# Kernel optimization log

Measured on AMD Instinct MI355X. Metric: run time of the kernel, lower is better.

Reference implementation:

```python
import jax, jax.numpy as jnp
import numpy as np

DIM = 192
NH = 6
HD = DIM // NH            # 32
SCALE = HD ** -0.5
HID = int(DIM * 4.0)      # 768
EPS = 1e-5


def _ln(x, g, b):
    m = jnp.mean(x, axis=-1, keepdims=True)
    v = jnp.mean((x - m) ** 2, axis=-1, keepdims=True)
    return (x - m) * jax.lax.rsqrt(v + EPS) * g + b


def setup_inputs() -> dict:
    key = jax.random.key(0)
    ks = jax.random.split(key, 6)
    H = W = T = 48
    B = 1
    L = H * W * T
    return {
        "x": jax.random.normal(ks[0], (B, L, DIM), jnp.float32),
        "norm1_g": jnp.ones((DIM,), jnp.float32),
        "norm1_b": jnp.zeros((DIM,), jnp.float32),
        "qkv_w": jax.random.normal(ks[1], (3 * DIM, DIM), jnp.float32) * 0.02,
        "qkv_b": jnp.zeros((3 * DIM,), jnp.float32),
        "proj_w": jax.random.normal(ks[2], (DIM, DIM), jnp.float32) * 0.02,
        "proj_b": jnp.zeros((DIM,), jnp.float32),
        "norm2_g": jnp.ones((DIM,), jnp.float32),
        "norm2_b": jnp.zeros((DIM,), jnp.float32),
        "fc1_w": jax.random.normal(ks[3], (HID, DIM), jnp.float32) * 0.02,
        "fc1_b": jnp.zeros((HID,), jnp.float32),
        "fc2_w": jax.random.normal(ks[4], (DIM, HID), jnp.float32) * 0.02,
        "fc2_b": jnp.zeros((DIM,), jnp.float32),
        "H": H, "W": W, "T": T,
    }


def reference(x, norm1_g, norm1_b, qkv_w, qkv_b, proj_w, proj_b,
              norm2_g, norm2_b, fc1_w, fc1_b, fc2_w, fc2_b, H, W, T):
    B, L, C = x.shape
    shortcut = x
    h = _ln(x, norm1_g, norm1_b)
    # axial_dims='12' -> extra_dim=3: permute to (B, T, H, W, C), attend over H*W
    h = h.reshape(B, H, W, T, C).transpose(0, 3, 1, 2, 4).reshape(B * T, H * W, C)
    B_, N, _ = h.shape
    qkv = h @ qkv_w.T + qkv_b                                   # (B_, N, 3C)
    # faithful reproduction of the module's unusual reshape mixing batch into head dim
    qkv = qkv.transpose(1, 0, 2).reshape(1, N, 3, NH, B_ * HD).transpose(2, 0, 3, 1, 4)
    q, k, v = qkv[0] * SCALE, qkv[1], qkv[2]                    # (1, NH, N, B_*HD)
    attn = jax.nn.softmax(jnp.einsum('ohnd,ohmd->ohnm', q, k), axis=-1)
    o = jnp.einsum('ohnm,ohmd->ohnd', attn, v)                  # (1, NH, N, B_*HD)
    o = o.transpose(0, 2, 1, 3).reshape(B_, N, C)
    o = o @ proj_w.T + proj_b
    o = o.reshape(B, H * W * T, C)                              # module does NOT undo the permute
    x1 = shortcut + o
    m = _ln(x1, norm2_g, norm2_b)
    m = jax.nn.gelu(m @ fc1_w.T + fc1_b, approximate=False) @ fc2_w.T + fc2_b
    return x1 + m
```

## Files before the change

### kernel.cpp

```cpp
#include <hip/hip_runtime.h>

typedef __bf16 bf16_t;
typedef __attribute__((ext_vector_type(8))) __bf16 bf16x8;
typedef __attribute__((ext_vector_type(4))) float f32x4;

__device__ __forceinline__ float gelu_exact(float x) {
    return 0.5f * x * (1.0f + erff(x * 0.70710678118654752f));
}

template<int BM, int BN, int EPI, int SWZ>
__global__ __launch_bounds__(256)
void mgemm(const bf16_t* __restrict__ A, int lda, long aBatch,
           const bf16_t* __restrict__ B, int ldb, long bBatch,
           bf16_t* __restrict__ C, int ldc, long cBatch,
           const float* __restrict__ bias, int K,
           float* __restrict__ Cf, const float* __restrict__ resid)
{
    constexpr int MR = BM / 32;
    constexpr int NR = BN / 32;
    constexpr int LPT = BM / 32 + BN / 32;
    __shared__ __align__(16) bf16_t As[2][BM * 64];
    __shared__ __align__(16) bf16_t Bs[2][BN * 64];
    const int t    = threadIdx.x;
    const int w    = t >> 6;
    const int lane = t & 63;
    const int wr   = w >> 1, wc = w & 1;

    unsigned bx = blockIdx.x, by = blockIdx.y, bz = blockIdx.z;
    if constexpr (SWZ) {
        const unsigned gx = gridDim.x, gy = gridDim.y, gz = gridDim.z;
        unsigned lin = (bz * gy + by) * gx + bx;
        const unsigned cpx = (gx * gy * gz) >> 3;
        lin = (lin & 7) * cpx + (lin >> 3);
        bx = lin % gx; lin /= gx;
        by = lin % gy; bz = lin / gy;
    }

    const long n0 = (long)bx * BN;
    const long m0 = (long)by * BM;
    A += (long)bz * aBatch;
    B += (long)bz * bBatch;
    if constexpr (EPI != 3) C += (long)bz * cBatch;

    f32x4 acc[MR][NR] = {};

    const int srow8  = t >> 3;
    const int schunk = (t & 7) ^ (srow8 & 7);
    const int lrow = lane & 15;
    const int kq4  = lane >> 4;

    auto stage = [&](int buf, int k0) {
        #pragma unroll
        for (int c = 0; c < BM / 32; ++c) {
            const bf16_t* src = A + (m0 + c * 32 + srow8) * (long)lda + (k0 + schunk * 8);
            __builtin_amdgcn_global_load_lds(
                (__attribute__((address_space(1))) void*)(bf16_t*)src,
                (__attribute__((address_space(3))) void*)(As[buf] + c * 2048 + w * 512),
                16, 0, 0);
        }
        #pragma unroll
        for (int c = 0; c < BN / 32; ++c) {
            const bf16_t* src = B + (n0 + c * 32 + srow8) * (long)ldb + (k0 + schunk * 8);
            __builtin_amdgcn_global_load_lds(
                (__attribute__((address_space(1))) void*)(bf16_t*)src,
                (__attribute__((address_space(3))) void*)(Bs[buf] + c * 2048 + w * 512),
                16, 0, 0);
        }
    };

    const int nt = K >> 6;
    stage(0, 0);
    int cur = 0;
    for (int kt = 0; kt < nt; ++kt) {
        if (kt + 1 < nt) {
            stage(cur ^ 1, (kt + 1) << 6);
            if constexpr (LPT == 8)
                asm volatile("s_waitcnt vmcnt(8)" ::: "memory");
            else
                asm volatile("s_waitcnt vmcnt(6)" ::: "memory");
        } else {
            asm volatile("s_waitcnt vmcnt(0)" ::: "memory");
        }
        __builtin_amdgcn_s_barrier();

        bf16x8 af[MR][2], bfr[NR][2];
        #pragma unroll
        for (int i = 0; i < MR; ++i) {
            const int row = wr * (BM / 2) + i * 16 + lrow;
            #pragma unroll
            for (int ks = 0; ks < 2; ++ks) {
                const int ch = (ks * 4 + kq4) ^ (row & 7);
                af[i][ks] = *(const bf16x8*)(As[cur] + row * 64 + ch * 8);
            }
        }
        #pragma unroll
        for (int j = 0; j < NR; ++j) {
            const int row = wc * (BN / 2) + j * 16 + lrow;
            #pragma unroll
            for (int ks = 0; ks < 2; ++ks) {
                const int ch = (ks * 4 + kq4) ^ (row & 7);
                bfr[j][ks] = *(const bf16x8*)(Bs[cur] + row * 64 + ch * 8);
            }
        }
        #pragma unroll
        for (int ks = 0; ks < 2; ++ks)
            #pragma unroll
            for (int i = 0; i < MR; ++i)
                #pragma unroll
                for (int j = 0; j < NR; ++j)
                    acc[i][j] = __builtin_amdgcn_mfma_f32_16x16x32_bf16(
                        af[i][ks], bfr[j][ks], acc[i][j], 0, 0, 0);

        asm volatile("s_waitcnt lgkmcnt(0)" ::: "memory");
        __builtin_amdgcn_s_barrier();
        cur ^= 1;
    }

    const int ccol  = lane & 15;
    const int crow4 = (lane >> 4) * 4;
    #pragma unroll
    for (int i = 0; i < MR; ++i) {
        long rowb = m0 + wr * (BM / 2) + i * 16 + crow4;
        #pragma unroll
        for (int j = 0; j < NR; ++j) {
            long col = n0 + wc * (BN / 2) + j * 16 + ccol;
            #pragma unroll
            for (int r = 0; r < 4; ++r) {
                float v = acc[i][j][r];
                long row = rowb + r;
                if constexpr (EPI == 0) {
                    C[row * ldc + col] = (bf16_t)v;
                } else if constexpr (EPI == 1) {
                    C[row * ldc + col] = (bf16_t)(v + bias[col]);
                } else if constexpr (EPI == 2) {
                    C[row * ldc + col] = (bf16_t)gelu_exact(v + bias[col]);
                } else {
                    long idx = row * ldc + col;
                    Cf[idx] = resid[idx] + v + bias[col];
                }
            }
        }
    }
}

__global__ __launch_bounds__(256)
void transpose_v(const bf16_t* __restrict__ Y, bf16_t* __restrict__ Vt)
{
    __shared__ bf16_t tile[64][80];
    const int h  = blockIdx.z;
    const int e0 = blockIdx.x * 64;
    const int m0 = blockIdx.y * 64;
    const int t  = threadIdx.x;
    const int lr = t >> 3;
    const int lc8 = t & 7;

    #pragma unroll
    for (int i = 0; i < 64; i += 32) {
        int row = lr + i;
        bf16x8 vv = *(const bf16x8*)(Y + (long)(m0 + row) * 27648 + 18432 + h * 1536 + e0 + lc8 * 8);
        int cs = lc8 ^ (row >> 3);
        *(bf16x8*)&tile[row][cs * 8] = vv;
    }
    __syncthreads();
    #pragma unroll
    for (int i = 0; i < 64; i += 32) {
        int er = lr + i;
        bf16x8 vv;
        #pragma unroll
        for (int j = 0; j < 8; ++j) {
            int row = lc8 * 8 + j;
            int cs = (er >> 3) ^ lc8;
            vv[j] = tile[row][cs * 8 + (er & 7)];
        }
        *(bf16x8*)(Vt + ((long)h * 1536 + e0 + er) * 2304 + m0 + lc8 * 8) = vv;
    }
}

__global__ __launch_bounds__(256)
void ln_fast(const float* __restrict__ x, const float* __restrict__ g,
             const float* __restrict__ b, bf16_t* __restrict__ o, int nrows)
{
    const int lane = threadIdx.x & 63;
    const int wave = threadIdx.x >> 6;
    const float g0 = g[lane], g1 = g[lane + 64], g2 = g[lane + 128];
    const float b0 = b[lane], b1 = b[lane + 64], b2 = b[lane + 128];
    for (long row = (long)blockIdx.x * 4 + wave; row < nrows; row += (long)gridDim.x * 4) {
        const float* xr = x + row * 192;
        float v0 = xr[lane], v1 = xr[lane + 64], v2 = xr[lane + 128];
        float s  = v0 + v1 + v2;
        float ss = v0 * v0 + v1 * v1 + v2 * v2;
        #pragma unroll
        for (int d = 32; d > 0; d >>= 1) {
            s  += __shfl_xor(s, d);
            ss += __shfl_xor(ss, d);
        }
        float mean = s * (1.f / 192.f);
        float var  = ss * (1.f / 192.f) - mean * mean;
        float rs   = rsqrtf(var + 1e-5f);
        bf16_t* orow = o + row * 192;
        orow[lane]       = (bf16_t)((v0 - mean) * rs * g0 + b0);
        orow[lane + 64]  = (bf16_t)((v1 - mean) * rs * g1 + b1);
        orow[lane + 128] = (bf16_t)((v2 - mean) * rs * g2 + b2);
    }
}

__global__ __launch_bounds__(256)
void softmax_fast(bf16_t* __restrict__ S)
{
    const float SC = 0.17677669529663687f;
    __shared__ float wmax[4], wsum[4];
    const long base = (long)blockIdx.x * 2304;
    const int t = threadIdx.x;
    const int lane = t & 63, w = t >> 6;
    float v[9];
    float mx = -1e30f;
    #pragma unroll
    for (int i = 0; i < 9; ++i) {
        v[i] = (float)S[base + t + i * 256] * SC;
        mx = fmaxf(mx, v[i]);
    }
    #pragma unroll
    for (int d = 32; d > 0; d >>= 1) mx = fmaxf(mx, __shfl_xor(mx, d));
    if (lane == 0) wmax[w] = mx;
    __syncthreads();
    mx = fmaxf(fmaxf(wmax[0], wmax[1]), fmaxf(wmax[2], wmax[3]));
    float sum = 0.f;
    #pragma unroll
    for (int i = 0; i < 9; ++i) { v[i] = __expf(v[i] - mx); sum += v[i]; }
    #pragma unroll
    for (int d = 32; d > 0; d >>= 1) sum += __shfl_xor(sum, d);
    if (lane == 0) wsum[w] = sum;
    __syncthreads();
    const float inv = 1.f / (wsum[0] + wsum[1] + wsum[2] + wsum[3]);
    #pragma unroll
    for (int i = 0; i < 9; ++i) S[base + t + i * 256] = (bf16_t)(v[i] * inv);
}

__global__ __launch_bounds__(256)
void cast_all(const float* __restrict__ w0, const float* __restrict__ w1,
              const float* __restrict__ w2, const float* __restrict__ w3,
              bf16_t* __restrict__ o0, bf16_t* __restrict__ o1,
              bf16_t* __restrict__ o2, bf16_t* __restrict__ o3)
{
    int i = blockIdx.x * 256 + threadIdx.x;
    if (i < 110592)       o0[i] = (bf16_t)w0[i];
    else if (i < 147456)  o1[i - 110592] = (bf16_t)w1[i - 110592];
    else if (i < 294912)  o2[i - 147456] = (bf16_t)w2[i - 147456];
    else if (i < 442368)  o3[i - 294912] = (bf16_t)w3[i - 294912];
}

extern "C" void kernel_launch(void* const* d_in, const int* in_sizes, int n_in,
                              void* d_out, int out_size, void* d_ws, size_t ws_size,
                              hipStream_t stream)
{
    (void)in_sizes; (void)n_in; (void)out_size; (void)ws_size;
    const float* x      = (const float*)d_in[0];
    const float* n1g    = (const float*)d_in[1];
    const float* n1b    = (const float*)d_in[2];
    const float* qkv_w  = (const float*)d_in[3];
    const float* qkv_b  = (const float*)d_in[4];
    const float* proj_w = (const float*)d_in[5];
    const float* proj_b = (const float*)d_in[6];
    const float* n2g    = (const float*)d_in[7];
    const float* n2b    = (const float*)d_in[8];
    const float* fc1_w  = (const float*)d_in[9];
    const float* fc1_b  = (const float*)d_in[10];
    const float* fc2_w  = (const float*)d_in[11];
    const float* fc2_b  = (const float*)d_in[12];
    float* out = (float*)d_out;

    char* ws = (char*)d_ws;
    size_t off = 0;
    auto alloc = [&](size_t nbytes) -> void* {
        off = (off + 255) & ~(size_t)255;
        void* p = ws + off;
        off += nbytes;
        return p;
    };

    bf16_t* Wq   = (bf16_t*)alloc((size_t)576 * 192 * 2);
    bf16_t* Wp   = (bf16_t*)alloc((size_t)192 * 192 * 2);
    bf16_t* W1   = (bf16_t*)alloc((size_t)768 * 192 * 2);
    bf16_t* W2   = (bf16_t*)alloc((size_t)192 * 768 * 2);
    bf16_t* Hbuf = (bf16_t*)alloc((size_t)110592 * 192 * 2);
    bf16_t* Qkv  = (bf16_t*)alloc((size_t)110592 * 768 * 2);
    bf16_t* Vt   = Qkv + (size_t)110592 * 576;
    bf16_t* Sbuf = (bf16_t*)d_out;

    cast_all<<<1728, 256, 0, stream>>>(qkv_w, proj_w, fc1_w, fc2_w, Wq, Wp, W1, W2);

    ln_fast<<<2048, 256, 0, stream>>>(x, n1g, n1b, Hbuf, 110592);
    mgemm<128, 64, 1, 0><<<dim3(9, 864, 1), 256, 0, stream>>>(
        Hbuf, 192, 0, Wq, 192, 0, Qkv, 576, 0, qkv_b, 192, nullptr, nullptr);
    transpose_v<<<dim3(24, 36, 6), 256, 0, stream>>>(Qkv, Vt);
    mgemm<128, 128, 0, 1><<<dim3(18, 18, 6), 256, 0, stream>>>(
        Qkv, 27648, 1536, Qkv + 9216, 27648, 1536,
        Sbuf, 2304, (long)2304 * 2304, nullptr, 1536, nullptr, nullptr);
    softmax_fast<<<13824, 256, 0, stream>>>(Sbuf);
    mgemm<128, 128, 0, 1><<<dim3(12, 18, 6), 256, 0, stream>>>(
        Sbuf, 2304, (long)2304 * 2304, Vt, 2304, (long)1536 * 2304,
        Hbuf, 9216, 1536, nullptr, 2304, nullptr, nullptr);
    mgemm<128, 64, 3, 0><<<dim3(3, 864, 1), 256, 0, stream>>>(
        Hbuf, 192, 0, Wp, 192, 0, nullptr, 192, 0, proj_b, 192, out, x);
    ln_fast<<<2048, 256, 0, stream>>>(out, n2g, n2b, Hbuf, 110592);
    mgemm<128, 128, 2, 0><<<dim3(6, 864, 1), 256, 0, stream>>>(
        Hbuf, 192, 0, W1, 192, 0, Qkv, 768, 0, fc1_b, 192, nullptr, nullptr);
    mgemm<128, 64, 3, 0><<<dim3(3, 864, 1), 256, 0, stream>>>(
        Qkv, 768, 0, W2, 768, 0, nullptr, 192, 0, fc2_b, 768, out, out);
}
```

Measured before the change: 792.2 us.

## Add 256x256-tile 512-thread GEMM for attention score and PV matmuls

Introduces a new GEMM kernel with 256x256 output tiles, 8 waves, 128 KB of dynamic LDS and a finer-grained half-tile staging pipeline with split barriers and MFMA priority boosts. It is used for the QK^T and attn·V batched matmuls, replacing the 128x128 mgemm. It also remaps workgroup IDs so consecutive tiles land on the same XCD. Larger tiles raise arithmetic intensity and cut global/L2 traffic, at the cost of lower occupancy and fewer workgroups (486 and 324) over the GPU's CUs, which can leave some CUs idle.

```diff
diff --git a/kernel.cpp b/kernel.cpp
--- a/kernel.cpp
+++ b/kernel.cpp
@@ -6,6 +6,144 @@
 
 __device__ __forceinline__ float gelu_exact(float x) {
     return 0.5f * x * (1.0f + erff(x * 0.70710678118654752f));
+}
+
+#define AS1 __attribute__((address_space(1)))
+#define AS3 __attribute__((address_space(3)))
+
+#define MM_HALF(IH)                                                            \
+    __builtin_amdgcn_s_setprio(1);                                             \
+    _Pragma("unroll")                                                          \
+    for (int u = 0; u < 4; ++u) {                                              \
+        _Pragma("unroll")                                                      \
+        for (int j = 0; j < 4; ++j)                                            \
+            acc[(IH) * 4 + u][j] = __builtin_amdgcn_mfma_f32_16x16x32_bf16(    \
+                a[u], b[j], acc[(IH) * 4 + u][j], 0, 0, 0);                    \
+    }                                                                          \
+    __builtin_amdgcn_s_setprio(0);
+
+#define MIDBAR()                                                \
+    asm volatile("" ::: "memory");                              \
+    __builtin_amdgcn_s_barrier();                               \
+    asm volatile("s_waitcnt lgkmcnt(0)" ::: "memory");
+
+#define ENDBAR()                                                \
+    asm volatile("" ::: "memory");                              \
+    __builtin_amdgcn_s_barrier();                               \
+    asm volatile("" ::: "memory");
+
+__global__ __launch_bounds__(512, 2)
+void gemm256(const bf16_t* __restrict__ A, int lda, long aBatch,
+             const bf16_t* __restrict__ B, int ldb, long bBatch,
+             bf16_t* __restrict__ C, int ldc, long cBatch, int K)
+{
+    extern __shared__ __align__(16) bf16_t lds[];
+    const int t    = threadIdx.x;
+    const int w    = t >> 6;
+    const int lane = t & 63;
+    const int wm   = w >> 2, wn = w & 3;
+    const int lrow = lane & 15;
+    const int kq4  = lane >> 4;
+
+    const unsigned gx = gridDim.x, gy = gridDim.y;
+    unsigned nwg = gx * gy * gridDim.z;
+    unsigned lin = (blockIdx.z * gy + blockIdx.y) * gx + blockIdx.x;
+    {
+        unsigned q = nwg >> 3, r = nwg & 7;
+        unsigned xcd = lin & 7, idx = lin >> 3;
+        lin = (xcd < r ? xcd * (q + 1) : r * (q + 1) + (xcd - r) * q) + idx;
+    }
+    const unsigned bx = lin % gx;
+    const unsigned by = (lin / gx) % gy;
+    const unsigned bz = lin / (gx * gy);
+
+    const long n0 = (long)bx * 256;
+    const long m0 = (long)by * 256;
+    const bf16_t* Ap = A + (long)bz * aBatch + m0 * lda;
+    const bf16_t* Bp = B + (long)bz * bBatch + n0 * ldb;
+    C += (long)bz * cBatch;
+
+    f32x4 acc[8][4] = {};
+
+    auto stage_half = [&](int buf, int op, int kh, int kt) {
+        const bf16_t* base = op ? Bp : Ap;
+        const int ld = op ? ldb : lda;
+        #pragma unroll
+        for (int e = 0; e < 2; ++e) {
+            const int row = e * 128 + (t >> 2);
+            const int cw  = (t & 3) ^ ((row ^ (row >> 2)) & 3);
+            const bf16_t* src = base + (long)row * ld + (kt * 64 + kh * 32 + cw * 8);
+            __builtin_amdgcn_global_load_lds(
+                (AS1 void*)(bf16_t*)src,
+                (AS3 void*)(lds + buf * 32768 + op * 16384 + kh * 8192 + e * 4096 + w * 512),
+                16, 0, 0);
+        }
+    };
+
+    bf16x8 a[4], b[4];
+    auto rdA = [&](int c, int ks, int ih) {
+        #pragma unroll
+        for (int u = 0; u < 4; ++u) {
+            const int row = wm * 128 + (ih * 4 + u) * 16 + lrow;
+            const int cw  = kq4 ^ ((row ^ (row >> 2)) & 3);
+            a[u] = *(const bf16x8*)(lds + c * 32768 + ks * 8192 + row * 32 + cw * 8);
+        }
+    };
+    auto rdB = [&](int c, int ks) {
+        #pragma unroll
+        for (int u = 0; u < 4; ++u) {
+            const int row = wn * 64 + u * 16 + lrow;
+            const int cw  = kq4 ^ ((row ^ (row >> 2)) & 3);
+            b[u] = *(const bf16x8*)(lds + c * 32768 + 16384 + ks * 8192 + row * 32 + cw * 8);
+        }
+    };
+
+    const int nt = K >> 6;
+    stage_half(0, 1, 0, 0); stage_half(0, 0, 0, 0);
+    stage_half(0, 1, 1, 0); stage_half(0, 0, 1, 0);
+    if (nt > 1) {
+        stage_half(1, 1, 0, 1); stage_half(1, 0, 0, 1); stage_half(1, 1, 1, 1);
+        asm volatile("s_waitcnt vmcnt(6)" ::: "memory");
+    } else {
+        asm volatile("s_waitcnt vmcnt(0)" ::: "memory");
+    }
+    __builtin_amdgcn_s_barrier();
+    asm volatile("" ::: "memory");
+
+    for (int kt = 0; kt < nt; ++kt) {
+        const int c = kt & 1;
+        rdA(c, 0, 0); rdB(c, 0);
+        if (kt + 1 < nt) stage_half(c ^ 1, 0, 1, kt + 1);
+        MIDBAR(); MM_HALF(0); ENDBAR();
+        rdA(c, 0, 1);
+        if (kt + 2 < nt) stage_half(c, 1, 0, kt + 2);
+        MIDBAR(); MM_HALF(1); ENDBAR();
+        rdA(c, 1, 0); rdB(c, 1);
+        if (kt + 2 < nt) stage_half(c, 0, 0, kt + 2);
+        MIDBAR(); MM_HALF(0); ENDBAR();
+        rdA(c, 1, 1);
+        if (kt + 2 < nt) {
+            stage_half(c, 1, 1, kt + 2);
+            asm volatile("s_waitcnt vmcnt(6)" ::: "memory");
+        } else {
+            asm volatile("s_waitcnt vmcnt(0)" ::: "memory");
+        }
+        MIDBAR(); MM_HALF(1); ENDBAR();
+    }
+
+    const int ccol  = lane & 15;
+    const int crow4 = (lane >> 4) * 4;
+    #pragma unroll
+    for (int i = 0; i < 8; ++i) {
+        long rowb = m0 + wm * 128 + i * 16 + crow4;
+        #pragma unroll
+        for (int j = 0; j < 4; ++j) {
+            long col = n0 + wn * 64 + j * 16 + ccol;
+            #pragma unroll
+            for (int r = 0; r < 4; ++r)
+                C[(rowb + r) * ldc + col] = (bf16_t)acc[i][j][r];
+        }
+    }
 }
 
 template<int BM, int BN, int EPI, int SWZ>
@@ -54,17 +192,15 @@
         for (int c = 0; c < BM / 32; ++c) {
             const bf16_t* src = A + (m0 + c * 32 + srow8) * (long)lda + (k0 + schunk * 8);
             __builtin_amdgcn_global_load_lds(
-                (__attribute__((address_space(1))) void*)(bf16_t*)src,
-                (__attribute__((address_space(3))) void*)(As[buf] + c * 2048 + w * 512),
-                16, 0, 0);
+                (AS1 void*)(bf16_t*)src,
+                (AS3 void*)(As[buf] + c * 2048 + w * 512), 16, 0, 0);
         }
         #pragma unroll
         for (int c = 0; c < BN / 32; ++c) {
             const bf16_t* src = B + (n0 + c * 32 + srow8) * (long)ldb + (k0 + schunk * 8);
             __builtin_amdgcn_global_load_lds(
-                (__attribute__((address_space(1))) void*)(bf16_t*)src,
-                (__attribute__((address_space(3))) void*)(Bs[buf] + c * 2048 + w * 512),
-                16, 0, 0);
+                (AS1 void*)(bf16_t*)src,
+                (AS3 void*)(Bs[buf] + c * 2048 + w * 512), 16, 0, 0);
         }
     };
 
@@ -287,19 +423,37 @@
     bf16_t* Vt   = Qkv + (size_t)110592 * 576;
     bf16_t* Sbuf = (bf16_t*)d_out;
 
+    static bool attrOk = []() {
+        return hipFuncSetAttribute(reinterpret_cast<const void*>(gemm256),
+                                   hipFuncAttributeMaxDynamicSharedMemorySize,
+                                   131072) == hipSuccess;
+    }();
+
     cast_all<<<1728, 256, 0, stream>>>(qkv_w, proj_w, fc1_w, fc2_w, Wq, Wp, W1, W2);
 
     ln_fast<<<2048, 256, 0, stream>>>(x, n1g, n1b, Hbuf, 110592);
     mgemm<128, 64, 1, 0><<<dim3(9, 864, 1), 256, 0, stream>>>(
         Hbuf, 192, 0, Wq, 192, 0, Qkv, 576, 0, qkv_b, 192, nullptr, nullptr);
     transpose_v<<<dim3(24, 36, 6), 256, 0, stream>>>(Qkv, Vt);
-    mgemm<128, 128, 0, 1><<<dim3(18, 18, 6), 256, 0, stream>>>(
-        Qkv, 27648, 1536, Qkv + 9216, 27648, 1536,
-        Sbuf, 2304, (long)2304 * 2304, nullptr, 1536, nullptr, nullptr);
+    if (attrOk) {
+        gemm256<<<dim3(9, 9, 6), 512, 131072, stream>>>(
+            Qkv, 27648, 1536, Qkv + 9216, 27648, 1536,
+            Sbuf, 2304, (long)2304 * 2304, 1536);
+    } else {
+        mgemm<128, 128, 0, 1><<<dim3(18, 18, 6), 256, 0, stream>>>(
+            Qkv, 27648, 1536, Qkv + 9216, 27648, 1536,
+            Sbuf, 2304, (long)2304 * 2304, nullptr, 1536, nullptr, nullptr);
+    }
     softmax_fast<<<13824, 256, 0, stream>>>(Sbuf);
-    mgemm<128, 128, 0, 1><<<dim3(12, 18, 6), 256, 0, stream>>>(
-        Sbuf, 2304, (long)2304 * 2304, Vt, 2304, (long)1536 * 2304,
-        Hbuf, 9216, 1536, nullptr, 2304, nullptr, nullptr);
+    if (attrOk) {
+        gemm256<<<dim3(6, 9, 6), 512, 131072, stream>>>(
+            Sbuf, 2304, (long)2304 * 2304, Vt, 2304, (long)1536 * 2304,
+            Hbuf, 9216, 1536, 2304);
+    } else {
+        mgemm<128, 128, 0, 1><<<dim3(12, 18, 6), 256, 0, stream>>>(
+            Sbuf, 2304, (long)2304 * 2304, Vt, 2304, (long)1536 * 2304,
+            Hbuf, 9216, 1536, nullptr, 2304, nullptr, nullptr);
+    }
     mgemm<128, 64, 3, 0><<<dim3(3, 864, 1), 256, 0, stream>>>(
         Hbuf, 192, 0, Wp, 192, 0, nullptr, 192, 0, proj_b, 192, out, x);
     ln_fast<<<2048, 256, 0, stream>>>(out, n2g, n2b, Hbuf, 110592);
```

Measured after the change: 789.9 us. About the same (-0.3%).
